# Optimization experiments

Hardware: AMD Instinct MI355X
Metric: run time of the kernel (lower is better)

## Reference

```python
import jax, jax.numpy as jnp
import numpy as np

DIM = 256
HEADS = 8
DIM_HEAD = 32
SLICE_NUM = 64
B, N = 4, 32768


def setup_inputs() -> dict:
    key = jax.random.key(0)
    ks = jax.random.split(key, 8)
    inner = HEADS * DIM_HEAD
    s = 0.02
    x = jax.random.normal(ks[0], (B, N, DIM), dtype=jnp.float32)
    Wx = jax.random.normal(ks[1], (inner, DIM), dtype=jnp.float32) * s
    bx = jnp.zeros((inner,), dtype=jnp.float32)
    Wfx = jax.random.normal(ks[2], (inner, DIM), dtype=jnp.float32) * s
    bfx = jnp.zeros((inner,), dtype=jnp.float32)
    # orthogonal init for in_project_slice (S x D)
    g = jax.random.normal(ks[3], (SLICE_NUM, DIM_HEAD), dtype=jnp.float32)
    q, _ = jnp.linalg.qr(g.T)  # D x min(D,S); S>D so orthogonal columns
    Wslice = jnp.concatenate([q.T, jax.random.normal(ks[4], (SLICE_NUM - DIM_HEAD, DIM_HEAD)) * s], axis=0)
    bslice = jnp.zeros((SLICE_NUM,), dtype=jnp.float32)
    Wqkv = jax.random.normal(ks[5], (3 * DIM_HEAD, DIM_HEAD), dtype=jnp.float32) * s
    Wout = jax.random.normal(ks[6], (DIM, inner), dtype=jnp.float32) * s
    bout = jnp.zeros((DIM,), dtype=jnp.float32)
    temperature = jnp.ones((1, 1, HEADS, 1), dtype=jnp.float32) * 0.5
    return {"x": x, "Wx": Wx, "bx": bx, "Wfx": Wfx, "bfx": bfx,
            "Wslice": Wslice, "bslice": bslice, "Wqkv": Wqkv,
            "Wout": Wout, "bout": bout, "temperature": temperature}


def reference(x, Wx, bx, Wfx, bfx, Wslice, bslice, Wqkv, Wout, bout, temperature):
    b, n, c = x.shape
    inner = Wx.shape[0]
    d = Wqkv.shape[1]           # dim_head
    h = inner // d              # heads
    s = Wslice.shape[0]         # slice_num
    # project_input_onto_slices (irregular-mesh, standard Transolver)
    x_mid = (x @ Wx.T + bx).reshape(b, n, h, d)
    fx = (x @ Wfx.T + bfx).reshape(b, n, h, d)
    proj = jnp.einsum('bnhd,sd->bnhs', x_mid, Wslice) + bslice  # (B,N,H,S)
    # temperature-scaled softmax over slices
    temp = jnp.clip(temperature, 0.5, 5.0)  # (1,1,H,1)
    slice_weights = jax.nn.softmax(proj / temp, axis=-1)
    # pool tokens -> slice tokens
    slice_norm = slice_weights.sum(axis=1) + 0.01  # (B,H,S)
    normed = slice_weights / slice_norm[:, None, :, :]
    slice_token = jnp.einsum('bnhs,bnhd->bhsd', normed, fx)
    # small attention among slices (SDPA, scale = d^-0.5)
    qkv = jnp.einsum('bhsd,ed->bhse', slice_token, Wqkv)  # e = 3d
    q, k, v = jnp.split(qkv, 3, axis=-1)
    attn = jax.nn.softmax(jnp.einsum('bhqd,bhkd->bhqk', q, k) * (d ** -0.5), axis=-1)
    out_tok = jnp.einsum('bhqk,bhkd->bhqd', attn, v)  # (B,H,S,D)
    # unslice back to tokens
    out_x = jnp.einsum('bnhs,bhsd->bnhd', slice_weights, out_tok).reshape(b, n, inner)
    return out_x @ Wout.T + bout
```

## Files before the change

### kernel.cpp

```cpp
#include <hip/hip_runtime.h>

#define NB 4
#define NTOK 32768
#define BNT 131072
#define CDIM 256
#define HH 8
#define NCOL 768

typedef _Float16 f16;
typedef __attribute__((ext_vector_type(8))) _Float16 f16x8;
typedef __attribute__((ext_vector_type(4))) _Float16 f16x4;
typedef __attribute__((ext_vector_type(4))) float f32x4;

__device__ inline void gload_lds16(const void* g, void* l) {
    __builtin_amdgcn_global_load_lds(
        (const __attribute__((address_space(1))) void*)g,
        (__attribute__((address_space(3))) void*)l, 16, 0, 0);
}

__global__ __launch_bounds__(256) void xcvt(
    const float* __restrict__ x, f16* __restrict__ xf)
{
    long i = (long)blockIdx.x * 256 + threadIdx.x;
    const long stride = (long)gridDim.x * 256;
    const long n4 = (long)BNT * CDIM / 4;
    for (; i < n4; i += stride) {
        float4 v = ((const float4*)x)[i];
        f16x4 o = {(f16)v.x, (f16)v.y, (f16)v.z, (f16)v.w};
        *(f16x4*)(xf + i * 4) = o;
    }
}

__global__ __launch_bounds__(256) void k0_build(
    const float* __restrict__ Wx, const float* __restrict__ bx,
    const float* __restrict__ Wfx, const float* __restrict__ bfx,
    const float* __restrict__ Wslice, const float* __restrict__ bslice,
    f16* __restrict__ Bt, float* __restrict__ bcomb)
{
    int col = blockIdx.x;
    int k = threadIdx.x;
    float acc;
    if (col < 256) {
        acc = Wfx[col * 256 + k];
        if (k == 0) bcomb[col] = bfx[col];
    } else {
        int p = col - 256, h = p >> 6, s = p & 63;
        acc = 0.f;
        #pragma unroll
        for (int d = 0; d < 32; ++d)
            acc += Wx[(h * 32 + d) * 256 + k] * Wslice[s * 32 + d];
        if (k == 0) {
            float bacc = bslice[s];
            #pragma unroll
            for (int d = 0; d < 32; ++d)
                bacc += bx[h * 32 + d] * Wslice[s * 32 + d];
            bcomb[col] = bacc;
        }
    }
    Bt[(long)col * 256 + k] = (f16)acc;
}

template<int NSO, bool FUSE_SM>
__global__ __launch_bounds__(512) void gemm_w(
    const f16* __restrict__ A, const f16* __restrict__ Bt,
    const float* __restrict__ bias, float* __restrict__ Cf,
    f16* __restrict__ Cfx, f16* __restrict__ Cw,
    const float* __restrict__ temperature, long bStrideB)
{
    constexpr int KO = NSO * 32;
    __shared__ char lds[73728];

    const int tid = threadIdx.x;
    const int lane = tid & 63;
    const int w = tid >> 6;
    const int wm = w >> 2, wn = w & 3;

    const int nx = gridDim.x;
    const int nwg = nx * gridDim.y;
    const int lid = blockIdx.y * nx + blockIdx.x;
    const int swz = (lid & 7) * (nwg >> 3) + (lid >> 3);
    const int m0 = (swz / nx) * 128, n0 = (swz % nx) * 256;

    const f16* BtB = Bt + ((long)m0 >> 15) * bStrideB;

    f32x4 acc[4][4] = {};

    auto stage = [&](int cs, int buf) {
        char* base = lds + buf * 24576;
        {
            int r = tid >> 2, c = tid & 3;
            int csrc = c ^ ((r >> 1) & 3);
            gload_lds16(A + (long)(m0 + r) * KO + cs * 32 + csrc * 8,
                        base + (tid & ~63) * 16);
        }
        #pragma unroll
        for (int i = 0; i < 2; ++i) {
            int q = (w * 2 + i) * 64 + lane;
            int r = q >> 2, c = q & 3;
            int csrc = c ^ ((r >> 1) & 3);
            gload_lds16(BtB + (long)(n0 + r) * KO + cs * 32 + csrc * 8,
                        base + 8192 + (w * 2 + i) * 1024);
        }
    };

    stage(0, 0);
    stage(1, 1);
    asm volatile("s_waitcnt vmcnt(3)" ::: "memory");
    __builtin_amdgcn_sched_barrier(0);
    __builtin_amdgcn_s_barrier();

    for (int cs = 0; cs < NSO; ++cs) {
        const int buf = cs % 3;
        if (cs + 2 < NSO) stage(cs + 2, (cs + 2) % 3);
        const char* sa = lds + buf * 24576;
        const char* sb = sa + 8192;
        const int cr = lane >> 4;
        f16x8 a[4], b[4];
        #pragma unroll
        for (int mi = 0; mi < 4; ++mi) {
            int r = wm * 64 + mi * 16 + (lane & 15);
            a[mi] = *(const f16x8*)(sa + r * 64 + ((cr ^ ((r >> 1) & 3)) << 4));
        }
        #pragma unroll
        for (int ni = 0; ni < 4; ++ni) {
            int r = wn * 64 + ni * 16 + (lane & 15);
            b[ni] = *(const f16x8*)(sb + r * 64 + ((cr ^ ((r >> 1) & 3)) << 4));
        }
        #pragma unroll
        for (int mi = 0; mi < 4; ++mi)
            #pragma unroll
            for (int ni = 0; ni < 4; ++ni)
                acc[mi][ni] = __builtin_amdgcn_mfma_f32_16x16x32_f16(
                    a[mi], b[ni], acc[mi][ni], 0, 0, 0);
        if (cs + 1 < NSO) {
            if (cs + 2 < NSO) asm volatile("s_waitcnt vmcnt(3)" ::: "memory");
            else              asm volatile("s_waitcnt vmcnt(0)" ::: "memory");
            __builtin_amdgcn_sched_barrier(0);
            __builtin_amdgcn_s_barrier();
        }
    }

    {
        int rbase = m0 + wm * 64 + (lane >> 4) * 4;
        int cbase = n0 + wn * 64 + (lane & 15);
        float bv[4];
        #pragma unroll
        for (int ni = 0; ni < 4; ++ni) bv[ni] = bias[cbase + ni * 16];

        if constexpr (FUSE_SM) {
            if (n0 > 0) {
                int h = ((n0 - 256) >> 6) + wn;
                float invt = 1.f / fminf(fmaxf(temperature[h], 0.5f), 5.0f);
                #pragma unroll
                for (int mi = 0; mi < 4; ++mi)
                    #pragma unroll
                    for (int rr = 0; rr < 4; ++rr) {
                        float v[4];
                        #pragma unroll
                        for (int ni = 0; ni < 4; ++ni)
                            v[ni] = (acc[mi][ni][rr] + bv[ni]) * invt;
                        float m = fmaxf(fmaxf(v[0], v[1]), fmaxf(v[2], v[3]));
                        #pragma unroll
                        for (int o = 1; o < 16; o <<= 1) m = fmaxf(m, __shfl_xor(m, o));
                        float e[4], ssum = 0.f;
                        #pragma unroll
                        for (int ni = 0; ni < 4; ++ni) { e[ni] = __expf(v[ni] - m); ssum += e[ni]; }
                        #pragma unroll
                        for (int o = 1; o < 16; o <<= 1) ssum += __shfl_xor(ssum, o);
                        float rs = 1.f / ssum;
                        long row = rbase + mi * 16 + rr;
                        #pragma unroll
                        for (int ni = 0; ni < 4; ++ni)
                            Cw[row * 512 + cbase + ni * 16 - 256] = (f16)(e[ni] * rs);
                    }
            } else {
                #pragma unroll
                for (int mi = 0; mi < 4; ++mi)
                    #pragma unroll
                    for (int rr = 0; rr < 4; ++rr) {
                        long row = rbase + mi * 16 + rr;
                        #pragma unroll
                        for (int ni = 0; ni < 4; ++ni)
                            Cfx[row * 256 + cbase + ni * 16] =
                                (f16)(acc[mi][ni][rr] + bv[ni]);
                    }
            }
        } else {
            #pragma unroll
            for (int mi = 0; mi < 4; ++mi)
                #pragma unroll
                for (int ni = 0; ni < 4; ++ni)
                    #pragma unroll
                    for (int rr = 0; rr < 4; ++rr)
                        Cf[(long)(rbase + mi * 16 + rr) * 256 + cbase + ni * 16] =
                            acc[mi][ni][rr] + bv[ni];
        }
    }
}

__global__ __launch_bounds__(256) void k1c_mfma(
    const f16* __restrict__ yfx, const f16* __restrict__ yw,
    float* __restrict__ partials)
{
    __shared__ char lds[49152];

    const int tid = threadIdx.x;
    const int lane = tid & 63;
    const int wv = tid >> 6;
    const int chunk64 = blockIdx.x & 63;
    const int bh = blockIdx.x >> 6;
    const int b = bh >> 3, h = bh & 7;
    const long tbase = (long)b * NTOK + (long)chunk64 * 512;

    f32x4 acc[4][3] = {};

    const f16 oe = ((lane & 15) == 0) ? (f16)1.0f : (f16)0.0f;
    const f16x8 bones = {oe, oe, oe, oe, oe, oe, oe, oe};
    const int g = lane >> 4;

    auto stage = [&](int iter, int buf) {
        const long t0 = tbase + iter * 128;
        char* base = lds + buf * 24576;
        #pragma unroll
        for (int i = 0; i < 4; ++i) {
            int k = wv * 4 + i;
            int sc = (lane & 7) ^ ((k & 3) << 1);
            gload_lds16(yw + (t0 + k * 8 + (lane >> 3)) * 512 + h * 64 + sc * 8,
                        base + k * 1024);
        }
        #pragma unroll
        for (int i = 0; i < 2; ++i) {
            int k = wv * 2 + i;
            int tq = (k & 1) * 16 + (lane >> 2);
            int dc = (lane & 3) ^ ((tq >> 3) & 3);
            gload_lds16(yfx + (t0 + k * 16 + (lane >> 2)) * 256 + h * 32 + dc * 8,
                        base + 16384 + k * 1024);
        }
    };

    stage(0, 0);
    for (int iter = 0; iter < 4; ++iter) {
        const int buf = iter & 1;
        if (iter < 3) {
            stage(iter + 1, buf ^ 1);
            asm volatile("s_waitcnt vmcnt(6)" ::: "memory");
        } else {
            asm volatile("s_waitcnt vmcnt(0)" ::: "memory");
        }
        __builtin_amdgcn_sched_barrier(0);
        const char* base = lds + buf * 24576;
        f16x8 a[4], bf[2];
        #pragma unroll
        for (int st = 0; st < 4; ++st) {
            int srow = st * 16 + (lane & 15);
            int schunk = (srow >> 3) ^ (g << 1);
            int off = wv * 4096 + g * 1024 + (schunk << 4) + (srow & 7) * 2;
            #pragma unroll
            for (int j = 0; j < 8; ++j)
                a[st][j] = *(const f16*)(base + off + j * 128);
        }
        #pragma unroll
        for (int dt = 0; dt < 2; ++dt) {
            int d = dt * 16 + (lane & 15);
            int dchunk = ((d >> 3) ^ g) & 3;
            int off = 16384 + wv * 2048 + g * 512 + (dchunk << 4) + (d & 7) * 2;
            #pragma unroll
            for (int j = 0; j < 8; ++j)
                bf[dt][j] = *(const f16*)(base + off + j * 64);
        }
        #pragma unroll
        for (int st = 0; st < 4; ++st) {
            acc[st][0] = __builtin_amdgcn_mfma_f32_16x16x32_f16(a[st], bf[0], acc[st][0], 0, 0, 0);
            acc[st][1] = __builtin_amdgcn_mfma_f32_16x16x32_f16(a[st], bf[1], acc[st][1], 0, 0, 0);
            acc[st][2] = __builtin_amdgcn_mfma_f32_16x16x32_f16(a[st], bones, acc[st][2], 0, 0, 0);
        }
    }
    __syncthreads();
    float* red = (float*)lds;
    #pragma unroll
    for (int st = 0; st < 4; ++st) {
        #pragma unroll
        for (int rr = 0; rr < 4; ++rr) {
            int s = st * 16 + g * 4 + rr;
            red[(wv * 64 + s) * 36 + (lane & 15)] = acc[st][0][rr];
            red[(wv * 64 + s) * 36 + 16 + (lane & 15)] = acc[st][1][rr];
            if ((lane & 15) == 0)
                red[(wv * 64 + s) * 36 + 32] = acc[st][2][rr];
        }
    }
    __syncthreads();
    float* P = partials + ((long)bh * 64 + chunk64) * 2112;
    for (int idx = tid; idx < 2112; idx += 256) {
        int s, c;
        if (idx < 2048) { s = idx >> 5; c = idx & 31; }
        else            { s = idx - 2048; c = 32; }
        float v = red[s * 36 + c] + red[(64 + s) * 36 + c]
                + red[(128 + s) * 36 + c] + red[(192 + s) * 36 + c];
        P[idx] = v;
    }
}

__global__ __launch_bounds__(256) void k3_slice(
    const float* __restrict__ partials,
    const float* __restrict__ Wqkv,
    const float* __restrict__ Wout,
    f16* __restrict__ OT2T)
{
    __shared__ float smem[14720];
    float* st = smem;
    float* q  = smem + 2112;
    float* kk = smem + 4224;
    float* v  = smem + 6336;
    float* L  = smem + 8448;
    float* red = L;
    float* ot = smem + 12608;

    int bh = blockIdx.x;
    int b = bh >> 3, h = bh & 7;
    int tid = threadIdx.x;

    for (int idx = tid; idx < 2112; idx += 256) {
        float s = 0.f;
        const float* P = partials + (long)bh * 64 * 2112 + idx;
        for (int c = 0; c < 64; ++c) s += P[c * 2112];
        red[idx] = s;
    }
    __syncthreads();
    for (int idx = tid; idx < 2048; idx += 256) {
        int s = idx >> 5, d = idx & 31;
        st[s * 33 + d] = red[idx] / (red[2048 + s] + 0.01f);
    }
    __syncthreads();
    for (int idx = tid; idx < 64 * 96; idx += 256) {
        int s = idx / 96, e = idx % 96;
        float acc = 0.f;
        #pragma unroll
        for (int d = 0; d < 32; ++d) acc += st[s * 33 + d] * Wqkv[e * 32 + d];
        if (e < 32)       q[s * 33 + e] = acc;
        else if (e < 64)  kk[s * 33 + (e - 32)] = acc;
        else              v[s * 33 + (e - 64)] = acc;
    }
    __syncthreads();
    for (int idx = tid; idx < 4096; idx += 256) {
        int i = idx >> 6, j = idx & 63;
        float acc = 0.f;
        #pragma unroll
        for (int d = 0; d < 32; ++d) acc += q[i * 33 + d] * kk[j * 33 + d];
        L[i * 65 + j] = acc * 0.17677669529663687f;
    }
    __syncthreads();
    {
        int lane = tid & 63, wid = tid >> 6;
        for (int r = wid; r < 64; r += 4) {
            float x = L[r * 65 + lane];
            float m = x;
            #pragma unroll
            for (int o = 32; o; o >>= 1) m = fmaxf(m, __shfl_xor(m, o));
            float e = __expf(x - m);
            float ss2 = e;
            #pragma unroll
            for (int o = 32; o; o >>= 1) ss2 += __shfl_xor(ss2, o);
            L[r * 65 + lane] = e / ss2;
        }
    }
    __syncthreads();
    for (int idx = tid; idx < 2048; idx += 256) {
        int s = idx >> 5, d = idx & 31;
        float acc = 0.f;
        #pragma unroll
        for (int j = 0; j < 64; ++j) acc += L[s * 65 + j] * v[j * 33 + d];
        ot[s * 33 + d] = acc;
    }
    __syncthreads();
    float* Wo = smem;
    for (int idx = tid; idx < 8192; idx += 256) {
        int c = idx >> 5, d = idx & 31;
        Wo[c * 33 + d] = Wout[c * 256 + h * 32 + d];
    }
    __syncthreads();
    {
        int c = tid;
        f16* O = OT2T + (long)b * 131072 + (long)c * 512 + h * 64;
        for (int s = 0; s < 64; ++s) {
            float acc = 0.f;
            #pragma unroll
            for (int d = 0; d < 32; ++d) acc += ot[s * 33 + d] * Wo[c * 33 + d];
            O[s] = (f16)acc;
        }
    }
}

extern "C" void kernel_launch(void* const* d_in, const int* in_sizes, int n_in,
                              void* d_out, int out_size, void* d_ws, size_t ws_size,
                              hipStream_t stream) {
    const float* x           = (const float*)d_in[0];
    const float* Wx          = (const float*)d_in[1];
    const float* bx          = (const float*)d_in[2];
    const float* Wfx         = (const float*)d_in[3];
    const float* bfx         = (const float*)d_in[4];
    const float* Wslice      = (const float*)d_in[5];
    const float* bslice      = (const float*)d_in[6];
    const float* Wqkv        = (const float*)d_in[7];
    const float* Wout        = (const float*)d_in[8];
    const float* bout        = (const float*)d_in[9];
    const float* temperature = (const float*)d_in[10];
    float* out = (float*)d_out;

    char* ws = (char*)d_ws;
    f16*   xf16     = (f16*)(ws);
    f16*   yfx      = (f16*)(ws + 67108864ULL);
    f16*   yw       = (f16*)(ws + 134217728ULL);
    float* partials = (float*)(ws + 268435456ULL);
    f16*   Bt       = (f16*)(ws + 285736960ULL);
    float* bcomb    = (float*)(ws + 286130176ULL);
    f16*   OT2T     = (f16*)(ws + 286133248ULL);

    k0_build<<<768, 256, 0, stream>>>(Wx, bx, Wfx, bfx, Wslice, bslice, Bt, bcomb);

    xcvt<<<2048, 256, 0, stream>>>(x, xf16);

    gemm_w<8, true><<<dim3(NCOL / 256, BNT / 128), 512, 0, stream>>>(
        xf16, Bt, bcomb, nullptr, yfx, yw, temperature, 0L);

    k1c_mfma<<<32 * 64, 256, 0, stream>>>(yfx, yw, partials);

    k3_slice<<<32, 256, 0, stream>>>(partials, Wqkv, Wout, OT2T);

    gemm_w<16, false><<<dim3(1, BNT / 128), 512, 0, stream>>>(
        yw, OT2T, bout, out, nullptr, nullptr, nullptr, 131072L);
}
```

Measured before the change: 358.2 us.

## Load GEMM B operand directly into registers and stage only A in LDS

New measurement: 453.1 us. 1.26x slower.

```diff
diff --git a/kernel.cpp b/kernel.cpp
--- a/kernel.cpp
+++ b/kernel.cpp
@@ -61,14 +61,14 @@
 }
 
 template<int NSO, bool FUSE_SM>
-__global__ __launch_bounds__(512) void gemm_w(
+__global__ __launch_bounds__(512) void gemm_breg(
     const f16* __restrict__ A, const f16* __restrict__ Bt,
     const float* __restrict__ bias, float* __restrict__ Cf,
     f16* __restrict__ Cfx, f16* __restrict__ Cw,
     const float* __restrict__ temperature, long bStrideB)
 {
     constexpr int KO = NSO * 32;
-    __shared__ char lds[73728];
+    __shared__ char lds[24576];
 
     const int tid = threadIdx.x;
     const int lane = tid & 63;
@@ -85,56 +85,45 @@
 
     f32x4 acc[4][4] = {};
 
-    auto stage = [&](int cs, int buf) {
-        char* base = lds + buf * 24576;
-        {
-            int r = tid >> 2, c = tid & 3;
-            int csrc = c ^ ((r >> 1) & 3);
-            gload_lds16(A + (long)(m0 + r) * KO + cs * 32 + csrc * 8,
-                        base + (tid & ~63) * 16);
-        }
-        #pragma unroll
-        for (int i = 0; i < 2; ++i) {
-            int q = (w * 2 + i) * 64 + lane;
-            int r = q >> 2, c = q & 3;
-            int csrc = c ^ ((r >> 1) & 3);
-            gload_lds16(BtB + (long)(n0 + r) * KO + cs * 32 + csrc * 8,
-                        base + 8192 + (w * 2 + i) * 1024);
-        }
+    auto stageA = [&](int cs, int buf) {
+        int r = tid >> 2, c = tid & 3;
+        int csrc = c ^ ((r >> 1) & 3);
+        gload_lds16(A + (long)(m0 + r) * KO + cs * 32 + csrc * 8,
+                    lds + buf * 8192 + (tid & ~63) * 16);
     };
 
-    stage(0, 0);
-    stage(1, 1);
-    asm volatile("s_waitcnt vmcnt(3)" ::: "memory");
+    stageA(0, 0);
+    stageA(1, 1);
+    asm volatile("s_waitcnt vmcnt(1)" ::: "memory");
     __builtin_amdgcn_sched_barrier(0);
     __builtin_amdgcn_s_barrier();
 
+    const int cr = lane >> 4;
+    #pragma unroll
     for (int cs = 0; cs < NSO; ++cs) {
-        const int buf = cs % 3;
-        if (cs + 2 < NSO) stage(cs + 2, (cs + 2) % 3);
-        const char* sa = lds + buf * 24576;
-        const char* sb = sa + 8192;
-        const int cr = lane >> 4;
-        f16x8 a[4], b[4];
+        if (cs + 2 < NSO) stageA(cs + 2, (cs + 2) % 3);
+        f16x8 b[4];
+        #pragma unroll
+        for (int ni = 0; ni < 4; ++ni) {
+            int rowb = n0 + wn * 64 + ni * 16 + (lane & 15);
+            b[ni] = *(const f16x8*)(BtB + (long)rowb * KO + cs * 32 + cr * 8);
+        }
+        const char* sa = lds + (cs % 3) * 8192;
+        f16x8 a[4];
         #pragma unroll
         for (int mi = 0; mi < 4; ++mi) {
             int r = wm * 64 + mi * 16 + (lane & 15);
             a[mi] = *(const f16x8*)(sa + r * 64 + ((cr ^ ((r >> 1) & 3)) << 4));
         }
-        #pragma unroll
-        for (int ni = 0; ni < 4; ++ni) {
-            int r = wn * 64 + ni * 16 + (lane & 15);
-            b[ni] = *(const f16x8*)(sb + r * 64 + ((cr ^ ((r >> 1) & 3)) << 4));
-        }
+        __builtin_amdgcn_s_setprio(1);
         #pragma unroll
         for (int mi = 0; mi < 4; ++mi)
             #pragma unroll
             for (int ni = 0; ni < 4; ++ni)
                 acc[mi][ni] = __builtin_amdgcn_mfma_f32_16x16x32_f16(
                     a[mi], b[ni], acc[mi][ni], 0, 0, 0);
+        __builtin_amdgcn_s_setprio(0);
         if (cs + 1 < NSO) {
-            if (cs + 2 < NSO) asm volatile("s_waitcnt vmcnt(3)" ::: "memory");
-            else              asm volatile("s_waitcnt vmcnt(0)" ::: "memory");
             __builtin_amdgcn_sched_barrier(0);
             __builtin_amdgcn_s_barrier();
         }
@@ -419,13 +408,13 @@
 
     xcvt<<<2048, 256, 0, stream>>>(x, xf16);
 
-    gemm_w<8, true><<<dim3(NCOL / 256, BNT / 128), 512, 0, stream>>>(
+    gemm_breg<8, true><<<dim3(NCOL / 256, BNT / 128), 512, 0, stream>>>(
         xf16, Bt, bcomb, nullptr, yfx, yw, temperature, 0L);
 
     k1c_mfma<<<32 * 64, 256, 0, stream>>>(yfx, yw, partials);
 
     k3_slice<<<32, 256, 0, stream>>>(partials, Wqkv, Wout, OT2T);
 
-    gemm_w<16, false><<<dim3(1, BNT / 128), 512, 0, stream>>>(
+    gemm_breg<16, false><<<dim3(1, BNT / 128), 512, 0, stream>>>(
         yw, OT2T, bout, out, nullptr, nullptr, nullptr, 131072L);
 }
```

## Fuse fp32-to-fp16 conversion of x into the projection GEMM A-load

Applied to the files above, without the earlier changes.

Measured after the change: 359.0 us. Within noise of the previous version (+0.2%).

```diff
diff --git a/kernel.cpp b/kernel.cpp
--- a/kernel.cpp
+++ b/kernel.cpp
@@ -16,19 +16,6 @@
     __builtin_amdgcn_global_load_lds(
         (const __attribute__((address_space(1))) void*)g,
         (__attribute__((address_space(3))) void*)l, 16, 0, 0);
-}
-
-__global__ __launch_bounds__(256) void xcvt(
-    const float* __restrict__ x, f16* __restrict__ xf)
-{
-    long i = (long)blockIdx.x * 256 + threadIdx.x;
-    const long stride = (long)gridDim.x * 256;
-    const long n4 = (long)BNT * CDIM / 4;
-    for (; i < n4; i += stride) {
-        float4 v = ((const float4*)x)[i];
-        f16x4 o = {(f16)v.x, (f16)v.y, (f16)v.z, (f16)v.w};
-        *(f16x4*)(xf + i * 4) = o;
-    }
 }
 
 __global__ __launch_bounds__(256) void k0_build(
@@ -60,12 +47,151 @@
     Bt[(long)col * 256 + k] = (f16)acc;
 }
 
-template<int NSO, bool FUSE_SM>
+template<int NSO>
+__global__ __launch_bounds__(512) void gemm_wx(
+    const float* __restrict__ A32, const f16* __restrict__ Bt,
+    const float* __restrict__ bias, f16* __restrict__ Cfx,
+    f16* __restrict__ Cw, const float* __restrict__ temperature)
+{
+    constexpr int KO = NSO * 32;
+    __shared__ char lds[73728];
+
+    const int tid = threadIdx.x;
+    const int lane = tid & 63;
+    const int w = tid >> 6;
+    const int wm = w >> 2, wn = w & 3;
+
+    const int nx = gridDim.x;
+    const int nwg = nx * gridDim.y;
+    const int lid = blockIdx.y * nx + blockIdx.x;
+    const int swz = (lid & 7) * (nwg >> 3) + (lid >> 3);
+    const int m0 = (swz / nx) * 128, n0 = (swz % nx) * 256;
+
+    f32x4 acc[4][4] = {};
+
+    const int ar = tid >> 2, ac = tid & 3;
+    const float* Asrc = A32 + (long)(m0 + ar) * CDIM + ac * 8;
+    const int aoff = ar * 64 + ((ac ^ ((ar >> 1) & 3)) << 4);
+
+    auto loadA = [&](int cs, float4& v0, float4& v1) {
+        v0 = *(const float4*)(Asrc + cs * 32);
+        v1 = *(const float4*)(Asrc + cs * 32 + 4);
+    };
+    auto writeA = [&](int buf, const float4& v0, const float4& v1) {
+        f16x8 o = {(f16)v0.x, (f16)v0.y, (f16)v0.z, (f16)v0.w,
+                   (f16)v1.x, (f16)v1.y, (f16)v1.z, (f16)v1.w};
+        *(f16x8*)(lds + buf * 24576 + aoff) = o;
+    };
+    auto stageB = [&](int cs, int buf) {
+        char* base = lds + buf * 24576;
+        #pragma unroll
+        for (int i = 0; i < 2; ++i) {
+            int q = (w * 2 + i) * 64 + lane;
+            int r = q >> 2, c = q & 3;
+            int csrc = c ^ ((r >> 1) & 3);
+            gload_lds16(Bt + (long)(n0 + r) * KO + cs * 32 + csrc * 8,
+                        base + 8192 + (w * 2 + i) * 1024);
+        }
+    };
+
+    {
+        float4 a0v0, a0v1, a1v0, a1v1;
+        loadA(0, a0v0, a0v1); stageB(0, 0);
+        loadA(1, a1v0, a1v1); stageB(1, 1);
+        writeA(0, a0v0, a0v1);
+        writeA(1, a1v0, a1v1);
+        asm volatile("s_waitcnt vmcnt(2) lgkmcnt(0)" ::: "memory");
+        __builtin_amdgcn_sched_barrier(0);
+        __builtin_amdgcn_s_barrier();
+    }
+
+    for (int cs = 0; cs < NSO; ++cs) {
+        const bool st = (cs + 2 < NSO);
+        float4 v0, v1;
+        if (st) { loadA(cs + 2, v0, v1); stageB(cs + 2, (cs + 2) % 3); }
+
+        const char* sa = lds + (cs % 3) * 24576;
+        const char* sb = sa + 8192;
+        const int cr = lane >> 4;
+        f16x8 a[4], b[4];
+        #pragma unroll
+        for (int mi = 0; mi < 4; ++mi) {
+            int r = wm * 64 + mi * 16 + (lane & 15);
+            a[mi] = *(const f16x8*)(sa + r * 64 + ((cr ^ ((r >> 1) & 3)) << 4));
+        }
+        #pragma unroll
+        for (int ni = 0; ni < 4; ++ni) {
+            int r = wn * 64 + ni * 16 + (lane & 15);
+            b[ni] = *(const f16x8*)(sb + r * 64 + ((cr ^ ((r >> 1) & 3)) << 4));
+        }
+        #pragma unroll
+        for (int mi = 0; mi < 4; ++mi)
+            #pragma unroll
+            for (int ni = 0; ni < 4; ++ni)
+                acc[mi][ni] = __builtin_amdgcn_mfma_f32_16x16x32_f16(
+                    a[mi], b[ni], acc[mi][ni], 0, 0, 0);
+
+        if (st) writeA((cs + 2) % 3, v0, v1);
+
+        if (cs + 1 < NSO) {
+            if (st) asm volatile("s_waitcnt vmcnt(2) lgkmcnt(0)" ::: "memory");
+            else    asm volatile("s_waitcnt vmcnt(0) lgkmcnt(0)" ::: "memory");
+            __builtin_amdgcn_sched_barrier(0);
+            __builtin_amdgcn_s_barrier();
+        }
+    }
+
+    {
+        int rbase = m0 + wm * 64 + (lane >> 4) * 4;
+        int cbase = n0 + wn * 64 + (lane & 15);
+        float bv[4];
+        #pragma unroll
+        for (int ni = 0; ni < 4; ++ni) bv[ni] = bias[cbase + ni * 16];
+
+        if (n0 > 0) {
+            int h = ((n0 - 256) >> 6) + wn;
+            float invt = 1.f / fminf(fmaxf(temperature[h], 0.5f), 5.0f);
+            #pragma unroll
+            for (int mi = 0; mi < 4; ++mi)
+                #pragma unroll
+                for (int rr = 0; rr < 4; ++rr) {
+                    float v[4];
+                    #pragma unroll
+                    for (int ni = 0; ni < 4; ++ni)
+                        v[ni] = (acc[mi][ni][rr] + bv[ni]) * invt;
+                    float m = fmaxf(fmaxf(v[0], v[1]), fmaxf(v[2], v[3]));
+                    #pragma unroll
+                    for (int o = 1; o < 16; o <<= 1) m = fmaxf(m, __shfl_xor(m, o));
+                    float e[4], ssum = 0.f;
+                    #pragma unroll
+                    for (int ni = 0; ni < 4; ++ni) { e[ni] = __expf(v[ni] - m); ssum += e[ni]; }
+                    #pragma unroll
+                    for (int o = 1; o < 16; o <<= 1) ssum += __shfl_xor(ssum, o);
+                    float rs = 1.f / ssum;
+                    long row = rbase + mi * 16 + rr;
+                    #pragma unroll
+                    for (int ni = 0; ni < 4; ++ni)
+                        Cw[row * 512 + cbase + ni * 16 - 256] = (f16)(e[ni] * rs);
+                }
+        } else {
+            #pragma unroll
+            for (int mi = 0; mi < 4; ++mi)
+                #pragma unroll
+                for (int rr = 0; rr < 4; ++rr) {
+                    long row = rbase + mi * 16 + rr;
+                    #pragma unroll
+                    for (int ni = 0; ni < 4; ++ni)
+                        Cfx[row * 256 + cbase + ni * 16] =
+                            (f16)(acc[mi][ni][rr] + bv[ni]);
+                }
+        }
+    }
+}
+
+template<int NSO>
 __global__ __launch_bounds__(512) void gemm_w(
     const f16* __restrict__ A, const f16* __restrict__ Bt,
-    const float* __restrict__ bias, float* __restrict__ Cf,
-    f16* __restrict__ Cfx, f16* __restrict__ Cw,
-    const float* __restrict__ temperature, long bStrideB)
+    const float* __restrict__ bias, float* __restrict__ Cf, long bStrideB)
 {
     constexpr int KO = NSO * 32;
     __shared__ char lds[73728];
@@ -146,55 +272,14 @@
         float bv[4];
         #pragma unroll
         for (int ni = 0; ni < 4; ++ni) bv[ni] = bias[cbase + ni * 16];
-
-        if constexpr (FUSE_SM) {
-            if (n0 > 0) {
-                int h = ((n0 - 256) >> 6) + wn;
-                float invt = 1.f / fminf(fmaxf(temperature[h], 0.5f), 5.0f);
+        #pragma unroll
+        for (int mi = 0; mi < 4; ++mi)
+            #pragma unroll
+            for (int ni = 0; ni < 4; ++ni)
                 #pragma unroll
-                for (int mi = 0; mi < 4; ++mi)
-                    #pragma unroll
-                    for (int rr = 0; rr < 4; ++rr) {
-                        float v[4];
-                        #pragma unroll
-                        for (int ni = 0; ni < 4; ++ni)
-                            v[ni] = (acc[mi][ni][rr] + bv[ni]) * invt;
-                        float m = fmaxf(fmaxf(v[0], v[1]), fmaxf(v[2], v[3]));
-                        #pragma unroll
-                        for (int o = 1; o < 16; o <<= 1) m = fmaxf(m, __shfl_xor(m, o));
-                        float e[4], ssum = 0.f;
-                        #pragma unroll
-                        for (int ni = 0; ni < 4; ++ni) { e[ni] = __expf(v[ni] - m); ssum += e[ni]; }
-                        #pragma unroll
-                        for (int o = 1; o < 16; o <<= 1) ssum += __shfl_xor(ssum, o);
-                        float rs = 1.f / ssum;
-                        long row = rbase + mi * 16 + rr;
-                        #pragma unroll
-                        for (int ni = 0; ni < 4; ++ni)
-                            Cw[row * 512 + cbase + ni * 16 - 256] = (f16)(e[ni] * rs);
-                    }
-            } else {
-                #pragma unroll
-                for (int mi = 0; mi < 4; ++mi)
-                    #pragma unroll
-                    for (int rr = 0; rr < 4; ++rr) {
-                        long row = rbase + mi * 16 + rr;
-                        #pragma unroll
-                        for (int ni = 0; ni < 4; ++ni)
-                            Cfx[row * 256 + cbase + ni * 16] =
-                                (f16)(acc[mi][ni][rr] + bv[ni]);
-                    }
-            }
-        } else {
-            #pragma unroll
-            for (int mi = 0; mi < 4; ++mi)
-                #pragma unroll
-                for (int ni = 0; ni < 4; ++ni)
-                    #pragma unroll
-                    for (int rr = 0; rr < 4; ++rr)
-                        Cf[(long)(rbase + mi * 16 + rr) * 256 + cbase + ni * 16] =
-                            acc[mi][ni][rr] + bv[ni];
-        }
+                for (int rr = 0; rr < 4; ++rr)
+                    Cf[(long)(rbase + mi * 16 + rr) * 256 + cbase + ni * 16] =
+                        acc[mi][ni][rr] + bv[ni];
     }
 }
 
@@ -407,25 +492,22 @@
     float* out = (float*)d_out;
 
     char* ws = (char*)d_ws;
-    f16*   xf16     = (f16*)(ws);
-    f16*   yfx      = (f16*)(ws + 67108864ULL);
-    f16*   yw       = (f16*)(ws + 134217728ULL);
-    float* partials = (float*)(ws + 268435456ULL);
-    f16*   Bt       = (f16*)(ws + 285736960ULL);
-    float* bcomb    = (float*)(ws + 286130176ULL);
-    f16*   OT2T     = (f16*)(ws + 286133248ULL);
+    f16*   yfx      = (f16*)(ws);
+    f16*   yw       = (f16*)(ws + 67108864ULL);
+    float* partials = (float*)(ws + 201326592ULL);
+    f16*   Bt       = (f16*)(ws + 218628096ULL);
+    float* bcomb    = (float*)(ws + 219021312ULL);
+    f16*   OT2T     = (f16*)(ws + 219024384ULL);
 
     k0_build<<<768, 256, 0, stream>>>(Wx, bx, Wfx, bfx, Wslice, bslice, Bt, bcomb);
 
-    xcvt<<<2048, 256, 0, stream>>>(x, xf16);
-
-    gemm_w<8, true><<<dim3(NCOL / 256, BNT / 128), 512, 0, stream>>>(
-        xf16, Bt, bcomb, nullptr, yfx, yw, temperature, 0L);
+    gemm_wx<8><<<dim3(NCOL / 256, BNT / 128), 512, 0, stream>>>(
+        x, Bt, bcomb, yfx, yw, temperature);
 
     k1c_mfma<<<32 * 64, 256, 0, stream>>>(yfx, yw, partials);
 
     k3_slice<<<32, 256, 0, stream>>>(partials, Wqkv, Wout, OT2T);
 
-    gemm_w<16, false><<<dim3(1, BNT / 128), 512, 0, stream>>>(
-        yw, OT2T, bout, out, nullptr, nullptr, nullptr, 131072L);
-}
+    gemm_w<16><<<dim3(1, BNT / 128), 512, 0, stream>>>(
+        yw, OT2T, bout, out, 131072L);
+}
```
